# Optimization experiments

Measured on AMD Instinct MI355X. Metric: run time of the kernel, lower is better.

The kernel has to match this reference:

```python
import jax, jax.numpy as jnp
import numpy as np

D_MODEL = 2048
N_HEADS = 16
N_KV = 4
D_K = D_MODEL // N_HEADS  # 128
B, T = 2, 2048


def setup_inputs() -> dict:
    key = jax.random.key(0)
    ks = jax.random.split(key, 10)
    s = 1.0 / np.sqrt(D_MODEL)
    x = jax.random.normal(ks[0], (B, T, D_MODEL), dtype=jnp.float32)
    mask = jnp.ones((B, 1, T, T), dtype=bool)
    Wq = jax.random.uniform(ks[1], (D_MODEL, D_MODEL), minval=-s, maxval=s, dtype=jnp.float32)
    bq = jax.random.uniform(ks[2], (D_MODEL,), minval=-s, maxval=s, dtype=jnp.float32)
    Wk = jax.random.uniform(ks[3], (D_MODEL, N_KV * D_K), minval=-s, maxval=s, dtype=jnp.float32)
    bk = jax.random.uniform(ks[4], (N_KV * D_K,), minval=-s, maxval=s, dtype=jnp.float32)
    Wv = jax.random.uniform(ks[5], (D_MODEL, N_KV * D_K), minval=-s, maxval=s, dtype=jnp.float32)
    bv = jax.random.uniform(ks[6], (N_KV * D_K,), minval=-s, maxval=s, dtype=jnp.float32)
    Wo = jax.random.uniform(ks[7], (D_MODEL, D_MODEL), minval=-s, maxval=s, dtype=jnp.float32)
    bo = jax.random.uniform(ks[8], (D_MODEL,), minval=-s, maxval=s, dtype=jnp.float32)
    return {"x": x, "mask": mask, "Wq": Wq, "bq": bq, "Wk": Wk, "bk": bk,
            "Wv": Wv, "bv": bv, "Wo": Wo, "bo": bo}


def reference(x, mask, Wq, bq, Wk, bk, Wv, bv, Wo, bo):
    Bn, Tn, _ = x.shape
    g = N_HEADS // N_KV
    # projections
    q = (x @ Wq + bq).reshape(Bn, Tn, N_HEADS, D_K).transpose(0, 2, 1, 3)  # [B,H,T,d]
    k = (x @ Wk + bk).reshape(Bn, Tn, N_KV, D_K).transpose(0, 2, 1, 3)     # [B,Hk,T,d]
    v = (x @ Wv + bv).reshape(Bn, Tn, N_KV, D_K).transpose(0, 2, 1, 3)
    # GQA broadcast: group Q heads as [B,Hk,g,T,d]; no repeat_interleave copy
    qg = q.reshape(Bn, N_KV, g, Tn, D_K)
    scores = jnp.einsum('bkgqd,bkld->bkgql', qg, k) / jnp.sqrt(jnp.float32(D_K))
    scores = jnp.where(mask[:, :, None, :, :], scores, jnp.float32(-1e9))
    attn = jax.nn.softmax(scores, axis=-1)  # dropout=0 (eval)
    out = jnp.einsum('bkgql,bkld->bkgqd', attn, v)  # [B,Hk,g,T,d]
    out = out.reshape(Bn, N_HEADS, Tn, D_K).transpose(0, 2, 1, 3).reshape(Bn, Tn, D_MODEL)
    return out @ Wo + bo
```

## Files before the change

kernel.cpp:

```cpp
#include <hip/hip_runtime.h>
#include <hip/hip_bf16.h>

typedef __attribute__((ext_vector_type(8))) short short8;
typedef __attribute__((ext_vector_type(4))) float f32x4;
typedef __attribute__((ext_vector_type(16))) float f32x16;
typedef __attribute__((ext_vector_type(2))) unsigned uint2v;

__device__ __forceinline__ unsigned short f2bf(float f) {
  union { float f; unsigned u; } v; v.f = f;
  unsigned u = v.u;
  return (unsigned short)((u + 0x7fffu + ((u >> 16) & 1u)) >> 16);
}

__device__ __forceinline__ unsigned packbf2(float a, float b) {
  union { __hip_bfloat162 h; unsigned u; } c;
  c.h = __float22bfloat162_rn(float2{a, b});
  return c.u;
}

__device__ __forceinline__ void gload16(void* lds, const void* g) {
  __builtin_amdgcn_global_load_lds(
      (__attribute__((address_space(1))) unsigned int*)g,
      (__attribute__((address_space(3))) unsigned int*)lds, 16, 0, 0);
}

#define BAR() asm volatile("s_barrier" ::: "memory")
#define LGKM0() asm volatile("s_waitcnt lgkmcnt(0)" ::: "memory")

__global__ void prep(const float* __restrict__ x, const float* __restrict__ Wq,
                     const float* __restrict__ Wk, const float* __restrict__ Wv,
                     const float* __restrict__ Wo,
                     unsigned short* __restrict__ xb,
                     unsigned short* __restrict__ wqkvT,
                     unsigned short* __restrict__ woT) {
  int id = blockIdx.x, tid = threadIdx.x;
  if (id < 4096) {
    int i = id * 256 + tid;
    const float4* p = (const float4*)x + (size_t)i * 2;
    float4 a = p[0], b = p[1];
    union { unsigned short u[8]; short8 v; } o;
    o.u[0] = f2bf(a.x); o.u[1] = f2bf(a.y); o.u[2] = f2bf(a.z); o.u[3] = f2bf(a.w);
    o.u[4] = f2bf(b.x); o.u[5] = f2bf(b.y); o.u[6] = f2bf(b.z); o.u[7] = f2bf(b.w);
    *(short8*)(xb + (size_t)i * 8) = o.v;
    return;
  }
  __shared__ float tile[32][33];
  const float* src; unsigned short* dst; int N, rowOff, tn, tk;
  if (id < 8192)       { int t = id - 4096;  src = Wq; dst = wqkvT; N = 2048; rowOff = 0;    tn = t & 63; tk = t >> 6; }
  else if (id < 9216)  { int t = id - 8192;  src = Wk; dst = wqkvT; N = 512;  rowOff = 2048; tn = t & 15; tk = t >> 4; }
  else if (id < 10240) { int t = id - 9216;  src = Wv; dst = wqkvT; N = 512;  rowOff = 2560; tn = t & 15; tk = t >> 4; }
  else                 { int t = id - 10240; src = Wo; dst = woT;   N = 2048; rowOff = 0;    tn = t & 63; tk = t >> 6; }
  int n0 = tn * 32, k0 = tk * 32;
  int c = tid & 31, rr = tid >> 5;
#pragma unroll
  for (int p = 0; p < 4; ++p) {
    int r = p * 8 + rr;
    tile[r][c] = src[(size_t)(k0 + r) * N + n0 + c];
  }
  __syncthreads();
#pragma unroll
  for (int p = 0; p < 4; ++p) {
    int r = p * 8 + rr;
    dst[(size_t)(rowOff + n0 + r) * 2048 + k0 + c] = f2bf(tile[c][r]);
  }
}

__global__ __launch_bounds__(512, 2) void gemm256(
    const unsigned short* __restrict__ A, const unsigned short* __restrict__ Bt,
    int K,
    const float* __restrict__ b0, const float* __restrict__ b1,
    const float* __restrict__ b2,
    unsigned short* __restrict__ oq, unsigned short* __restrict__ ok,
    unsigned short* __restrict__ ov) {
  __shared__ char L[131072];
  int tid = threadIdx.x, wid = tid >> 6, lane = tid & 63, lo = lane & 15, hi = lane >> 4;
  int wr = wid >> 2, wc = wid & 3;
  int m0 = blockIdx.x * 256, n0 = blockIdx.y * 256;
  const char* Ab = (const char*)A + (size_t)m0 * K * 2;
  const char* Bb = (const char*)Bt + (size_t)n0 * K * 2;
  f32x4 acc[8][4] = {};
  int NT = K >> 6;

  auto STAGE = [&](int p, int which, int kt) {
    const char* src = which ? Bb : Ab;
    char* dstb = L + p * 65536 + which * 32768 + wid * 1024;
#pragma unroll
    for (int it = 0; it < 4; ++it) {
      int o = it * 8192 + wid * 1024 + lane * 16;
      int r = o >> 7;
      int cb = (o & 127) ^ ((r & 7) << 4);
      gload16(dstb + it * 8192, src + (size_t)r * K * 2 + kt * 128 + cb);
    }
  };
  auto STAGE1 = [&](int p, int which, int kt, int c) {
    const char* src = which ? Bb : Ab;
    int o = c * 1024 + lane * 16;
    int r = o >> 7;
    int cb = (o & 127) ^ ((r & 7) << 4);
    gload16(L + p * 65536 + which * 32768 + c * 1024,
            src + (size_t)r * K * 2 + kt * 128 + cb);
  };

  short8 af[2][4], bf0[2][2], bf1[2][2];

  STAGE(0, 0, 0); STAGE(0, 1, 0);
  STAGE(1, 0, 1); STAGE(1, 1, 1);
  asm volatile("s_waitcnt vmcnt(8)" ::: "memory");
  BAR();

  for (int t = 0; t < NT; ++t) {
    int p = t & 1;
    const char* AB = L + p * 65536;
    const char* BB = AB + 32768;

#pragma unroll
    for (int ks = 0; ks < 2; ++ks) {
#pragma unroll
      for (int i = 0; i < 4; ++i) {
        int row = wr * 128 + i * 16 + lo;
        af[ks][i] = *(const short8*)(AB + ((row * 128 + ks * 64 + hi * 16) ^ ((row & 7) << 4)));
      }
#pragma unroll
      for (int j = 0; j < 2; ++j) {
        int row = wc * 64 + j * 16 + lo;
        bf0[ks][j] = *(const short8*)(BB + ((row * 128 + ks * 64 + hi * 16) ^ ((row & 7) << 4)));
      }
    }
    BAR(); LGKM0();
    __builtin_amdgcn_s_setprio(1);
#pragma unroll
    for (int ks = 0; ks < 2; ++ks)
#pragma unroll
      for (int i = 0; i < 4; ++i)
#pragma unroll
        for (int j = 0; j < 2; ++j)
          acc[i][j] = __builtin_amdgcn_mfma_f32_16x16x32_bf16(af[ks][i], bf0[ks][j], acc[i][j], 0, 0, 0);
    __builtin_amdgcn_s_setprio(0);
    BAR();

#pragma unroll
    for (int ks = 0; ks < 2; ++ks)
#pragma unroll
      for (int j = 0; j < 2; ++j) {
        int row = wc * 64 + 32 + j * 16 + lo;
        bf1[ks][j] = *(const short8*)(BB + ((row * 128 + ks * 64 + hi * 16) ^ ((row & 7) << 4)));
      }
    if (t + 2 < NT) { STAGE1(p, 0, t + 2, wid); STAGE1(p, 0, t + 2, 16 + wid); }
    BAR(); LGKM0();
    __builtin_amdgcn_s_setprio(1);
#pragma unroll
    for (int ks = 0; ks < 2; ++ks)
#pragma unroll
      for (int i = 0; i < 4; ++i)
#pragma unroll
        for (int j = 0; j < 2; ++j)
          acc[i][2 + j] = __builtin_amdgcn_mfma_f32_16x16x32_bf16(af[ks][i], bf1[ks][j], acc[i][2 + j], 0, 0, 0);
    __builtin_amdgcn_s_setprio(0);
    BAR();

#pragma unroll
    for (int ks = 0; ks < 2; ++ks)
#pragma unroll
      for (int i = 0; i < 4; ++i) {
        int row = wr * 128 + 64 + i * 16 + lo;
        af[ks][i] = *(const short8*)(AB + ((row * 128 + ks * 64 + hi * 16) ^ ((row & 7) << 4)));
      }
    if (t + 2 < NT) { STAGE1(p, 1, t + 2, 2 * wid); STAGE1(p, 1, t + 2, 2 * wid + 1); }
    BAR(); LGKM0();
    __builtin_amdgcn_s_setprio(1);
#pragma unroll
    for (int ks = 0; ks < 2; ++ks)
#pragma unroll
      for (int i = 0; i < 4; ++i)
#pragma unroll
        for (int j = 0; j < 2; ++j)
          acc[4 + i][2 + j] = __builtin_amdgcn_mfma_f32_16x16x32_bf16(af[ks][i], bf1[ks][j], acc[4 + i][2 + j], 0, 0, 0);
    __builtin_amdgcn_s_setprio(0);
    BAR();

    if (t + 2 < NT) {
      STAGE1(p, 0, t + 2, 8 + wid);  STAGE1(p, 0, t + 2, 24 + wid);
      STAGE1(p, 1, t + 2, 16 + 2 * wid); STAGE1(p, 1, t + 2, 17 + 2 * wid);
    }
    BAR();
    __builtin_amdgcn_s_setprio(1);
#pragma unroll
    for (int ks = 0; ks < 2; ++ks)
#pragma unroll
      for (int i = 0; i < 4; ++i)
#pragma unroll
        for (int j = 0; j < 2; ++j)
          acc[4 + i][j] = __builtin_amdgcn_mfma_f32_16x16x32_bf16(af[ks][i], bf0[ks][j], acc[4 + i][j], 0, 0, 0);
    __builtin_amdgcn_s_setprio(0);
    if (t == NT - 2) { asm volatile("s_waitcnt vmcnt(0)" ::: "memory"); }
    else             { asm volatile("s_waitcnt vmcnt(8)" ::: "memory"); }
    BAR();
  }

#pragma unroll
  for (int ii = 0; ii < 8; ++ii) {
    int mbase = m0 + wr * 128 + ii * 16 + hi * 4;
#pragma unroll
    for (int jj = 0; jj < 4; ++jj) {
      int n = n0 + wc * 64 + jj * 16 + lo;
      float bias;
      if (n < 2048) bias = b0[n];
      else if (n < 2560) bias = b1[n - 2048];
      else bias = b2[n - 2560];
#pragma unroll
      for (int r = 0; r < 4; ++r) {
        int mm = mbase + r;
        int b = mm >> 11, t = mm & 2047;
        float val = acc[ii][jj][r] + bias;
        if (n < 2048) {
          int h = n >> 7, d = n & 127;
          oq[(((size_t)(b * 16 + h)) * 2048 + t) * 128 + d] =
              f2bf(val * (0.08838834764831845f * 1.4426950408889634f));
        } else if (n < 2560) {
          int kvh = (n - 2048) >> 7, d = (n - 2048) & 127;
          ok[(((size_t)(b * 4 + kvh)) * 2048 + t) * 128 + d] = f2bf(val);
        } else {
          int kvh = (n - 2560) >> 7, d = (n - 2560) & 127;
          ov[(((size_t)(b * 4 + kvh)) * 128 + d) * 2048 + t] = f2bf(val);
        }
      }
    }
  }
}

__global__ __launch_bounds__(512, 2) void gemmO(
    const unsigned short* __restrict__ A, const unsigned short* __restrict__ Bt,
    int K, const float* __restrict__ bias, float* __restrict__ of) {
  __shared__ char L[98304];
  int tid = threadIdx.x, wid = tid >> 6, lane = tid & 63, lo = lane & 15, hi = lane >> 4;
  int wr = wid >> 2, wc = wid & 3;
  int m0 = blockIdx.x * 128, n0 = blockIdx.y * 256;
  const char* Ab = (const char*)A + (size_t)m0 * K * 2;
  const char* Bb = (const char*)Bt + (size_t)n0 * K * 2;
  f32x4 acc[4][4] = {};
  int NT = K >> 6;

  auto SA = [&](int p, int kt, int c) {
    int o = c * 1024 + lane * 16;
    int r = o >> 7;
    int cb = (o & 127) ^ ((r & 7) << 4);
    gload16(L + p * 49152 + c * 1024, Ab + (size_t)r * K * 2 + kt * 128 + cb);
  };
  auto SB = [&](int p, int kt, int c) {
    int o = c * 1024 + lane * 16;
    int r = o >> 7;
    int cb = (o & 127) ^ ((r & 7) << 4);
    gload16(L + p * 49152 + 16384 + c * 1024, Bb + (size_t)r * K * 2 + kt * 128 + cb);
  };
  int ev0 = (wid & 3) + (wid >> 2) * 8, ev1 = 16 + ev0;
  int od0 = 4 + (wid & 3) + (wid >> 2) * 8, od1 = 16 + od0;

  SA(0, 0, 2 * wid); SA(0, 0, 2 * wid + 1);
  SB(0, 0, ev0); SB(0, 0, ev1); SB(0, 0, od0); SB(0, 0, od1);
  SA(1, 1, 2 * wid); SA(1, 1, 2 * wid + 1); SB(1, 1, ev0); SB(1, 1, ev1);
  asm volatile("s_waitcnt vmcnt(4)" ::: "memory");
  BAR();

  for (int t = 0; t < NT; ++t) {
    int p = t & 1;
    const char* AB = L + p * 49152;
    const char* BB = AB + 16384;
    short8 af[2][4], bf0[2][2], bf1[2][2];

#pragma unroll
    for (int ks = 0; ks < 2; ++ks) {
#pragma unroll
      for (int i = 0; i < 4; ++i) {
        int row = wr * 64 + i * 16 + lo;
        af[ks][i] = *(const short8*)(AB + ((row * 128 + ks * 64 + hi * 16) ^ ((row & 7) << 4)));
      }
#pragma unroll
      for (int j = 0; j < 2; ++j) {
        int row = wc * 64 + j * 16 + lo;
        bf0[ks][j] = *(const short8*)(BB + ((row * 128 + ks * 64 + hi * 16) ^ ((row & 7) << 4)));
      }
    }
    if (t + 1 < NT) { SB(p ^ 1, t + 1, od0); SB(p ^ 1, t + 1, od1); }
    BAR(); LGKM0();
    __builtin_amdgcn_s_setprio(1);
#pragma unroll
    for (int ks = 0; ks < 2; ++ks)
#pragma unroll
      for (int i = 0; i < 4; ++i)
#pragma unroll
        for (int j = 0; j < 2; ++j)
          acc[i][j] = __builtin_amdgcn_mfma_f32_16x16x32_bf16(af[ks][i], bf0[ks][j], acc[i][j], 0, 0, 0);
    __builtin_amdgcn_s_setprio(0);
    if (t >= NT - 3) { asm volatile("s_waitcnt vmcnt(0)" ::: "memory"); }
    else             { asm volatile("s_waitcnt vmcnt(6)" ::: "memory"); }
    BAR();

#pragma unroll
    for (int ks = 0; ks < 2; ++ks)
#pragma unroll
      for (int j = 0; j < 2; ++j) {
        int row = wc * 64 + 32 + j * 16 + lo;
        bf1[ks][j] = *(const short8*)(BB + ((row * 128 + ks * 64 + hi * 16) ^ ((row & 7) << 4)));
      }
    if (t + 2 < NT) {
      SA(p, t + 2, 2 * wid); SA(p, t + 2, 2 * wid + 1);
      SB(p, t + 2, ev0); SB(p, t + 2, ev1);
    }
    BAR(); LGKM0();
    __builtin_amdgcn_s_setprio(1);
#pragma unroll
    for (int ks = 0; ks < 2; ++ks)
#pragma unroll
      for (int i = 0; i < 4; ++i)
#pragma unroll
        for (int j = 0; j < 2; ++j)
          acc[i][2 + j] = __builtin_amdgcn_mfma_f32_16x16x32_bf16(af[ks][i], bf1[ks][j], acc[i][2 + j], 0, 0, 0);
    __builtin_amdgcn_s_setprio(0);
    if (t >= NT - 3) { asm volatile("s_waitcnt vmcnt(0)" ::: "memory"); }
    else             { asm volatile("s_waitcnt vmcnt(6)" ::: "memory"); }
    BAR();
  }

#pragma unroll
  for (int ii = 0; ii < 4; ++ii) {
    int mbase = m0 + wr * 64 + ii * 16 + hi * 4;
#pragma unroll
    for (int jj = 0; jj < 4; ++jj) {
      int n = n0 + wc * 64 + jj * 16 + lo;
      float bv = bias[n];
#pragma unroll
      for (int r = 0; r < 4; ++r)
        of[(size_t)(mbase + r) * 2048 + n] = acc[ii][jj][r] + bv;
    }
  }
}

__device__ __forceinline__ void stageK(char* KLb, const char* kcb, int w, int lane, int t0) {
#pragma unroll
  for (int j = 0; j < 4; ++j) {
    int o = j * 4096 + w * 1024 + lane * 16;
    int row = o >> 8, col = o & 255;
    gload16(KLb + j * 4096 + w * 1024,
            kcb + (size_t)(t0 + row) * 256 + (col ^ ((row & 15) << 4)));
  }
}
__device__ __forceinline__ void stageV(char* VLb, const char* vcb, int w, int lane, int t0) {
#pragma unroll
  for (int j = 0; j < 4; ++j) {
    int o = j * 4096 + w * 1024 + lane * 16;
    int d = o >> 7, col = o & 127;
    gload16(VLb + j * 4096 + w * 1024,
            vcb + (size_t)d * 4096 + t0 * 2 + (col ^ ((d & 7) << 4)));
  }
}

__global__ __launch_bounds__(256, 2) void attn_fwd(
    const unsigned short* __restrict__ q, const unsigned short* __restrict__ kg,
    const unsigned short* __restrict__ vtg, unsigned short* __restrict__ attn) {
  __shared__ unsigned short kbuf[16384];
  __shared__ unsigned short vbuf[16384];
  int tid = threadIdx.x, w = tid >> 6, lane = tid & 63;
  int l31 = lane & 31, hi5 = lane >> 5;
  int tq0 = blockIdx.x * 128, h = blockIdx.y, b = blockIdx.z, kvh = h >> 2;
  int qrow = tq0 + w * 32;

  const unsigned short* qbase = q + ((size_t)(b * 16 + h)) * 2048 * 128;
  short8 qf[8];
#pragma unroll
  for (int ds_ = 0; ds_ < 8; ++ds_)
    qf[ds_] = *(const short8*)(qbase + (size_t)(qrow + l31) * 128 + ds_ * 16 + hi5 * 8);

  f32x16 oacc[4] = {};
  f32x16 lacc = {};
  float mrow = -1e30f;
  const short8 onesv = {16256, 16256, 16256, 16256, 16256, 16256, 16256, 16256};

  const char* kcb = (const char*)(kg + ((size_t)(b * 4 + kvh)) * 2048 * 128);
  const char* vcb = (const char*)(vtg + ((size_t)(b * 4 + kvh)) * 128 * 2048);
  char* KL = (char*)kbuf;
  char* VL = (char*)vbuf;

  stageK(KL, kcb, w, lane, 0);
  stageV(VL, vcb, w, lane, 0);
  __syncthreads();
  int buf = 0;

  for (int t0 = 0; t0 < 2048; t0 += 64) {
    if (t0 + 64 < 2048) {
      stageK(KL + (buf ^ 1) * 16384, kcb, w, lane, t0 + 64);
      stageV(VL + (buf ^ 1) * 16384, vcb, w, lane, t0 + 64);
    }
    const char* KB = KL + buf * 16384;
    const char* VB = VL + buf * 16384;

    f32x16 s[2] = {};
    __builtin_amdgcn_s_setprio(1);
#pragma unroll
    for (int ds_ = 0; ds_ < 8; ++ds_) {
#pragma unroll
      for (int f = 0; f < 2; ++f) {
        int row = f * 32 + l31;
        short8 kf = *(const short8*)(KB + ((row * 256 + ds_ * 32 + hi5 * 16) ^ ((row & 15) << 4)));
        s[f] = __builtin_amdgcn_mfma_f32_32x32x16_bf16(kf, qf[ds_], s[f], 0, 0, 0);
      }
    }
    __builtin_amdgcn_s_setprio(0);

    float am = fmaxf(s[0][0], s[0][1]);
#pragma unroll
    for (int r = 2; r < 14; r += 2) am = fmaxf(fmaxf(am, s[0][r]), s[0][r + 1]);
    am = fmaxf(fmaxf(am, s[0][14]), s[0][15]);
#pragma unroll
    for (int r = 0; r < 16; r += 2) am = fmaxf(fmaxf(am, s[1][r]), s[1][r + 1]);

    if (!__all(am <= mrow + 8.f)) {
      float ar = fmaxf(am, __shfl_xor(am, 32));
      float mnew = fmaxf(mrow, ar);
      float fsv = __builtin_amdgcn_exp2f(mrow - mnew);
      mrow = mnew;
#pragma unroll
      for (int g = 0; g < 4; ++g)
#pragma unroll
        for (int r = 0; r < 4; ++r) {
          float fsr = __shfl(fsv, r + 8 * g + 4 * hi5);
          lacc[4 * g + r] *= fsr;
#pragma unroll
          for (int db = 0; db < 4; ++db) oacc[db][4 * g + r] *= fsr;
        }
    }

    unsigned pk01[2][4], pk23[2][4];
#pragma unroll
    for (int f = 0; f < 2; ++f)
#pragma unroll
      for (int g = 0; g < 4; ++g) {
        float p0 = __builtin_amdgcn_exp2f(s[f][4 * g + 0] - mrow);
        float p1 = __builtin_amdgcn_exp2f(s[f][4 * g + 1] - mrow);
        float p2 = __builtin_amdgcn_exp2f(s[f][4 * g + 2] - mrow);
        float p3 = __builtin_amdgcn_exp2f(s[f][4 * g + 3] - mrow);
        pk01[f][g] = packbf2(p0, p1);
        pk23[f][g] = packbf2(p2, p3);
      }

    short8 pA[4];
#pragma unroll
    for (int f = 0; f < 2; ++f)
#pragma unroll
      for (int p = 0; p < 2; ++p) {
        uint2v a01 = __builtin_amdgcn_permlane32_swap(pk01[f][2 * p], pk01[f][2 * p + 1], false, false);
        uint2v a23 = __builtin_amdgcn_permlane32_swap(pk23[f][2 * p], pk23[f][2 * p + 1], false, false);
        union { unsigned u[4]; short8 v; } pa;
        pa.u[0] = a01.x; pa.u[1] = a23.x; pa.u[2] = a01.y; pa.u[3] = a23.y;
        pA[2 * f + p] = pa.v;
      }

    __builtin_amdgcn_s_setprio(1);
#pragma unroll
    for (int db = 0; db < 4; ++db) {
      int d = db * 32 + l31;
      int sw = (d & 7) << 4;
#pragma unroll
      for (int step = 0; step < 4; ++step) {
        short8 vf = *(const short8*)(VB + ((d * 128 + step * 32 + hi5 * 16) ^ sw));
        oacc[db] = __builtin_amdgcn_mfma_f32_32x32x16_bf16(pA[step], vf, oacc[db], 0, 0, 0);
      }
    }
#pragma unroll
    for (int step = 0; step < 4; ++step)
      lacc = __builtin_amdgcn_mfma_f32_32x32x16_bf16(pA[step], onesv, lacc, 0, 0, 0);
    __builtin_amdgcn_s_setprio(0);
    __syncthreads();
    buf ^= 1;
  }

  unsigned short* ob = attn + ((size_t)b * 2048) * 2048 + h * 128;
#pragma unroll
  for (int g = 0; g < 4; ++g)
#pragma unroll
    for (int r = 0; r < 4; ++r) {
      float lr = 1.0f / lacc[4 * g + r];
      int t = qrow + r + 8 * g + 4 * hi5;
#pragma unroll
      for (int db = 0; db < 4; ++db)
        ob[(size_t)t * 2048 + db * 32 + l31] = f2bf(oacc[db][4 * g + r] * lr);
    }
}

extern "C" void kernel_launch(void* const* d_in, const int* in_sizes, int n_in,
                              void* d_out, int out_size, void* d_ws, size_t ws_size,
                              hipStream_t stream) {
  const float* x  = (const float*)d_in[0];
  const float* Wq = (const float*)d_in[2];
  const float* bq = (const float*)d_in[3];
  const float* Wk = (const float*)d_in[4];
  const float* bk = (const float*)d_in[5];
  const float* Wv = (const float*)d_in[6];
  const float* bv = (const float*)d_in[7];
  const float* Wo = (const float*)d_in[8];
  const float* bo = (const float*)d_in[9];
  float* out = (float*)d_out;

  char* ws = (char*)d_ws;
  unsigned short* xb    = (unsigned short*)(ws);
  unsigned short* wqkvT = (unsigned short*)(ws + 16777216);
  unsigned short* woT   = (unsigned short*)(ws + 29360128);
  unsigned short* qb    = (unsigned short*)(ws + 37748736);
  unsigned short* kbw   = (unsigned short*)(ws + 54525952);
  unsigned short* vtw   = (unsigned short*)(ws + 58720256);
  unsigned short* attnb = (unsigned short*)(ws + 62914560);

  prep<<<dim3(14336), dim3(256), 0, stream>>>(x, Wq, Wk, Wv, Wo, xb, wqkvT, woT);

  gemm256<<<dim3(16, 12), dim3(512), 0, stream>>>(
      xb, wqkvT, 2048, bq, bk, bv, qb, kbw, vtw);

  attn_fwd<<<dim3(16, 16, 2), dim3(256), 0, stream>>>(qb, kbw, vtw, attnb);

  gemmO<<<dim3(32, 8), dim3(512), 0, stream>>>(attnb, woT, 2048, bo, out);
}
```

Measured before the change: 224.8 us.

## Shrink QKV GEMM tile to 64x256 for more blocks and restructure pipeline

Replaces the 256x256-tile QKV projection GEMM with a 64x256 tile kernel, launching 768 blocks instead of 192 so all compute units get work. The LDS double-buffer is resized to 40KB per stage and the load schedule is reworked with per-wave A/B chunk assignments and new vmcnt waits. The trade-off is lower arithmetic intensity per block and more redundant global reads of the weight matrix.

Result: faster. 208.3 us (-7.3%).

```diff
diff --git a/kernel.cpp b/kernel.cpp
--- a/kernel.cpp
+++ b/kernel.cpp
@@ -65,59 +65,54 @@
   }
 }
 
-__global__ __launch_bounds__(512, 2) void gemm256(
+__global__ __launch_bounds__(512, 4) void gemm64(
     const unsigned short* __restrict__ A, const unsigned short* __restrict__ Bt,
     int K,
     const float* __restrict__ b0, const float* __restrict__ b1,
     const float* __restrict__ b2,
     unsigned short* __restrict__ oq, unsigned short* __restrict__ ok,
     unsigned short* __restrict__ ov) {
-  __shared__ char L[131072];
+  __shared__ char L[81920];
   int tid = threadIdx.x, wid = tid >> 6, lane = tid & 63, lo = lane & 15, hi = lane >> 4;
   int wr = wid >> 2, wc = wid & 3;
-  int m0 = blockIdx.x * 256, n0 = blockIdx.y * 256;
+  int m0 = blockIdx.x * 64, n0 = blockIdx.y * 256;
   const char* Ab = (const char*)A + (size_t)m0 * K * 2;
   const char* Bb = (const char*)Bt + (size_t)n0 * K * 2;
-  f32x4 acc[8][4] = {};
+  f32x4 acc[2][4] = {};
   int NT = K >> 6;
 
-  auto STAGE = [&](int p, int which, int kt) {
-    const char* src = which ? Bb : Ab;
-    char* dstb = L + p * 65536 + which * 32768 + wid * 1024;
-#pragma unroll
-    for (int it = 0; it < 4; ++it) {
-      int o = it * 8192 + wid * 1024 + lane * 16;
-      int r = o >> 7;
-      int cb = (o & 127) ^ ((r & 7) << 4);
-      gload16(dstb + it * 8192, src + (size_t)r * K * 2 + kt * 128 + cb);
-    }
-  };
-  auto STAGE1 = [&](int p, int which, int kt, int c) {
-    const char* src = which ? Bb : Ab;
+  auto SA = [&](int p, int kt, int c) {
     int o = c * 1024 + lane * 16;
     int r = o >> 7;
     int cb = (o & 127) ^ ((r & 7) << 4);
-    gload16(L + p * 65536 + which * 32768 + c * 1024,
-            src + (size_t)r * K * 2 + kt * 128 + cb);
+    gload16(L + p * 40960 + c * 1024, Ab + (size_t)r * K * 2 + kt * 128 + cb);
   };
-
-  short8 af[2][4], bf0[2][2], bf1[2][2];
-
-  STAGE(0, 0, 0); STAGE(0, 1, 0);
-  STAGE(1, 0, 1); STAGE(1, 1, 1);
-  asm volatile("s_waitcnt vmcnt(8)" ::: "memory");
+  auto SB = [&](int p, int kt, int c) {
+    int o = c * 1024 + lane * 16;
+    int r = o >> 7;
+    int cb = (o & 127) ^ ((r & 7) << 4);
+    gload16(L + p * 40960 + 8192 + c * 1024, Bb + (size_t)r * K * 2 + kt * 128 + cb);
+  };
+  int ev0 = (wid & 3) + (wid >> 2) * 8, ev1 = 16 + ev0;
+  int od0 = 4 + (wid & 3) + (wid >> 2) * 8, od1 = 16 + od0;
+
+  SA(0, 0, wid);
+  SB(0, 0, ev0); SB(0, 0, ev1); SB(0, 0, od0); SB(0, 0, od1);
+  SA(1, 1, wid); SB(1, 1, ev0); SB(1, 1, ev1);
+  asm volatile("s_waitcnt vmcnt(3)" ::: "memory");
   BAR();
 
   for (int t = 0; t < NT; ++t) {
     int p = t & 1;
-    const char* AB = L + p * 65536;
-    const char* BB = AB + 32768;
+    const char* AB = L + p * 40960;
+    const char* BB = AB + 8192;
+    short8 af[2][2], bf0[2][2], bf1[2][2];
 
 #pragma unroll
     for (int ks = 0; ks < 2; ++ks) {
 #pragma unroll
-      for (int i = 0; i < 4; ++i) {
-        int row = wr * 128 + i * 16 + lo;
+      for (int i = 0; i < 2; ++i) {
+        int row = wr * 32 + i * 16 + lo;
         af[ks][i] = *(const short8*)(AB + ((row * 128 + ks * 64 + hi * 16) ^ ((row & 7) << 4)));
       }
 #pragma unroll
@@ -126,16 +121,19 @@
         bf0[ks][j] = *(const short8*)(BB + ((row * 128 + ks * 64 + hi * 16) ^ ((row & 7) << 4)));
       }
     }
+    if (t + 1 < NT) { SB(p ^ 1, t + 1, od0); SB(p ^ 1, t + 1, od1); }
     BAR(); LGKM0();
     __builtin_amdgcn_s_setprio(1);
 #pragma unroll
     for (int ks = 0; ks < 2; ++ks)
 #pragma unroll
-      for (int i = 0; i < 4; ++i)
+      for (int i = 0; i < 2; ++i)
 #pragma unroll
         for (int j = 0; j < 2; ++j)
           acc[i][j] = __builtin_amdgcn_mfma_f32_16x16x32_bf16(af[ks][i], bf0[ks][j], acc[i][j], 0, 0, 0);
     __builtin_amdgcn_s_setprio(0);
+    if (t >= NT - 3) { asm volatile("s_waitcnt vmcnt(0)" ::: "memory"); }
+    else             { asm volatile("s_waitcnt vmcnt(5)" ::: "memory"); }
     BAR();
 
 #pragma unroll
@@ -145,61 +143,25 @@
         int row = wc * 64 + 32 + j * 16 + lo;
         bf1[ks][j] = *(const short8*)(BB + ((row * 128 + ks * 64 + hi * 16) ^ ((row & 7) << 4)));
       }
-    if (t + 2 < NT) { STAGE1(p, 0, t + 2, wid); STAGE1(p, 0, t + 2, 16 + wid); }
+    if (t + 2 < NT) { SA(p, t + 2, wid); SB(p, t + 2, ev0); SB(p, t + 2, ev1); }
     BAR(); LGKM0();
     __builtin_amdgcn_s_setprio(1);
 #pragma unroll
     for (int ks = 0; ks < 2; ++ks)
 #pragma unroll
-      for (int i = 0; i < 4; ++i)
+      for (int i = 0; i < 2; ++i)
 #pragma unroll
         for (int j = 0; j < 2; ++j)
           acc[i][2 + j] = __builtin_amdgcn_mfma_f32_16x16x32_bf16(af[ks][i], bf1[ks][j], acc[i][2 + j], 0, 0, 0);
     __builtin_amdgcn_s_setprio(0);
+    if (t >= NT - 3) { asm volatile("s_waitcnt vmcnt(0)" ::: "memory"); }
+    else             { asm volatile("s_waitcnt vmcnt(5)" ::: "memory"); }
     BAR();
-
-#pragma unroll
-    for (int ks = 0; ks < 2; ++ks)
-#pragma unroll
-      for (int i = 0; i < 4; ++i) {
-        int row = wr * 128 + 64 + i * 16 + lo;
-        af[ks][i] = *(const short8*)(AB + ((row * 128 + ks * 64 + hi * 16) ^ ((row & 7) << 4)));
-      }
-    if (t + 2 < NT) { STAGE1(p, 1, t + 2, 2 * wid); STAGE1(p, 1, t + 2, 2 * wid + 1); }
-    BAR(); LGKM0();
-    __builtin_amdgcn_s_setprio(1);
-#pragma unroll
-    for (int ks = 0; ks < 2; ++ks)
-#pragma unroll
-      for (int i = 0; i < 4; ++i)
-#pragma unroll
-        for (int j = 0; j < 2; ++j)
-          acc[4 + i][2 + j] = __builtin_amdgcn_mfma_f32_16x16x32_bf16(af[ks][i], bf1[ks][j], acc[4 + i][2 + j], 0, 0, 0);
-    __builtin_amdgcn_s_setprio(0);
-    BAR();
-
-    if (t + 2 < NT) {
-      STAGE1(p, 0, t + 2, 8 + wid);  STAGE1(p, 0, t + 2, 24 + wid);
-      STAGE1(p, 1, t + 2, 16 + 2 * wid); STAGE1(p, 1, t + 2, 17 + 2 * wid);
-    }
-    BAR();
-    __builtin_amdgcn_s_setprio(1);
-#pragma unroll
-    for (int ks = 0; ks < 2; ++ks)
-#pragma unroll
-      for (int i = 0; i < 4; ++i)
-#pragma unroll
-        for (int j = 0; j < 2; ++j)
-          acc[4 + i][j] = __builtin_amdgcn_mfma_f32_16x16x32_bf16(af[ks][i], bf0[ks][j], acc[4 + i][j], 0, 0, 0);
-    __builtin_amdgcn_s_setprio(0);
-    if (t == NT - 2) { asm volatile("s_waitcnt vmcnt(0)" ::: "memory"); }
-    else             { asm volatile("s_waitcnt vmcnt(8)" ::: "memory"); }
-    BAR();
-  }
-
-#pragma unroll
-  for (int ii = 0; ii < 8; ++ii) {
-    int mbase = m0 + wr * 128 + ii * 16 + hi * 4;
+  }
+
+#pragma unroll
+  for (int ii = 0; ii < 2; ++ii) {
+    int mbase = m0 + wr * 32 + ii * 16 + hi * 4;
 #pragma unroll
     for (int jj = 0; jj < 4; ++jj) {
       int n = n0 + wc * 64 + jj * 16 + lo;
@@ -511,7 +473,7 @@
 
   prep<<<dim3(14336), dim3(256), 0, stream>>>(x, Wq, Wk, Wv, Wo, xb, wqkvT, woT);
 
-  gemm256<<<dim3(16, 12), dim3(512), 0, stream>>>(
+  gemm64<<<dim3(64, 12), dim3(512), 0, stream>>>(
       xb, wqkvT, 2048, bq, bk, bv, qb, kbw, vtw);
 
   attn_fwd<<<dim3(16, 16, 2), dim3(256), 0, stream>>>(qb, kbw, vtw, attnb);
```
